# Kernel tuning notes

Hardware: AMD Instinct MI355X
Metric: run time of the kernel (lower is better)

## Reference

```python
import jax, jax.numpy as jnp
import numpy as np

B, Q, K, H = 8, 2048, 2048, 512


def setup_inputs() -> dict:
    key = jax.random.key(0)
    ks = jax.random.split(key, 12)
    s = 1.0 / np.sqrt(H)
    return {
        "query": jax.random.normal(ks[0], (B, Q, H), jnp.float32),
        "key_": jax.random.normal(ks[1], (B, K, H), jnp.float32),
        "value": jax.random.normal(ks[2], (B, K, H), jnp.float32),
        "mask": jax.random.randint(ks[3], (B, K), 0, 2).astype(bool),
        "Wq": jax.random.normal(ks[4], (H, H), jnp.float32) * s,
        "bq": jnp.zeros((H,), jnp.float32),
        "Wk": jax.random.normal(ks[5], (H, H), jnp.float32) * s,
        "bk": jnp.zeros((H,), jnp.float32),
        "Wv": jax.random.normal(ks[6], (H, H), jnp.float32) * s,
        "bv": jnp.zeros((H,), jnp.float32),
        "Wo": jax.random.normal(ks[7], (H, H), jnp.float32) * s,
        "bo": jnp.zeros((H,), jnp.float32),
    }


def reference(query, key_, value, mask, Wq, bq, Wk, bk, Wv, bv, Wo, bo):
    scale = jnp.sqrt(jnp.float32(H))
    Qp = query @ Wq + bq          # (B,Q,H)
    Kp = key_ @ Wk + bk           # (B,K,H)
    Vp = value @ Wv + bv          # (B,K,H)
    energy = jnp.einsum("bqh,bkh->bqk", Qp, Kp) / scale
    # mask is (B, key_len); torch code broadcasts it over all query rows
    energy = jnp.where(mask[:, None, :], -jnp.inf, energy)
    idx = jnp.argmax(energy, axis=-1)                 # (B,Q)
    score = jax.nn.one_hot(idx, K, dtype=energy.dtype)  # hardmax one-hot (B,Q,K)
    # score @ V is exactly a per-row gather of the argmax-selected V row
    res = jnp.take_along_axis(Vp, idx[:, :, None], axis=1)  # (B,Q,H)
    res = res @ Wo + bo
    return (res, score)
```

## Files before the change

### kernel.cpp

```cpp
#include <hip/hip_runtime.h>

typedef _Float16 f16;
typedef f16 f16x8 __attribute__((ext_vector_type(8)));
typedef f16 f16x4 __attribute__((ext_vector_type(4)));
typedef short s16x8 __attribute__((ext_vector_type(8)));
typedef short s16x4 __attribute__((ext_vector_type(4)));
typedef float f32x4 __attribute__((ext_vector_type(4)));

#define MFMA16(a,b,c)  __builtin_amdgcn_mfma_f32_16x16x32_f16(a,b,c,0,0,0)
#define MFMAB16(a,b,c) __builtin_amdgcn_mfma_f32_16x16x32_bf16(a,b,c,0,0,0)

static constexpr int Bn = 8, Qn = 2048, Kn = 2048, Hn = 512;
static constexpr int Mn = Bn * Qn;

typedef __attribute__((address_space(1))) const unsigned int as1_uint;
typedef __attribute__((address_space(3))) unsigned int as3_uint;

__device__ __forceinline__ void gl_lds16(const void* g, void* l) {
    __builtin_amdgcn_global_load_lds((as1_uint*)g, (as3_uint*)l, 16, 0, 0);
}

__device__ __forceinline__ short bf16r(float x) {
    unsigned u = __builtin_bit_cast(unsigned, x);
    u += 0x7fffu + ((u >> 16) & 1u);
    return (short)(u >> 16);
}

__device__ __forceinline__ int swz(int row) { return (row >> 1) & 3; }

__global__ __launch_bounds__(256) void prep_all(
    const int* __restrict__ mask, const float* __restrict__ Wk,
    const float* __restrict__ Wo, const float* __restrict__ bq,
    const float* __restrict__ bv, const float* __restrict__ bo,
    int* __restrict__ cidx, int* __restrict__ cnt,
    f16* __restrict__ Wk_h, f16* __restrict__ Wk_l, short* __restrict__ Wot,
    float* __restrict__ wvec, float* __restrict__ cvec)
{
    const int bid = blockIdx.x, t = threadIdx.x;
    if (bid < 8) {
        __shared__ int sums[256];
        int b = bid;
        int base = b * Kn + t * 8;
        int mv[8]; int s = 0;
        #pragma unroll
        for (int i = 0; i < 8; ++i) { mv[i] = (mask[base + i] == 0); s += mv[i]; }
        sums[t] = s;
        __syncthreads();
        for (int off = 1; off < 256; off <<= 1) {
            int v = (t >= off) ? sums[t - off] : 0;
            __syncthreads();
            sums[t] += v;
            __syncthreads();
        }
        int pos = (t > 0 ? sums[t - 1] : 0);
        #pragma unroll
        for (int i = 0; i < 8; ++i)
            if (mv[i]) cidx[b * Kn + pos++] = t * 8 + i;
        if (t == 255) {
            int total = sums[255];
            if (total == 0) { cidx[b * Kn] = 0; total = 1; }
            cnt[b] = total;
        }
    } else if (bid < 1032) {
        int e = (bid - 8) * 256 + t;
        float v = Wk[e] * 512.0f;
        f16 h = (f16)v;
        Wk_h[e] = h; Wk_l[e] = (f16)((v - (float)h) * 2048.0f);
        int r = e >> 9, c = e & 511;
        Wot[c * 512 + r] = bf16r(Wo[e]);
    } else {
        #pragma unroll
        for (int i = 0; i < 2; ++i) {
            int tt = t + i * 256;
            float s = 0.f;
            for (int n = 0; n < 512; n += 4) {
                f32x4 a = *(const f32x4*)(Wk + (size_t)tt * 512 + n);
                f32x4 q = *(const f32x4*)(bq + n);
                s += a[0]*q[0] + a[1]*q[1] + a[2]*q[2] + a[3]*q[3];
            }
            wvec[tt] = s * (1.0f / 512.0f);
            float s2 = 0.f;
            for (int h = 0; h < 512; ++h) s2 += bv[h] * Wo[h * 512 + tt];
            cvec[tt] = s2 + bo[tt];
        }
    }
}

template<int PREP>
__global__ __launch_bounds__(256) void gemm_split(
    const float* __restrict__ Af,
    const f16* __restrict__ Bh_g, const f16* __restrict__ Bl_g,
    f16* __restrict__ Oh, f16* __restrict__ Ol)
{
    __shared__ __align__(16) f16 Ah[2][2048], Al[2][2048], Bh[2][4096], Bl[2][4096];
    const int tid = threadIdx.x, lane = tid & 63, wid = tid >> 6;
    const int l15 = lane & 15, lg = lane >> 4;
    const int m0 = blockIdx.x * 64, n0 = blockIdx.y * 128;
    const int srow = lane >> 2, sg = lane & 3;
    const int ar0 = tid >> 3, ac0 = (tid & 7) * 4;

    auto stageB = [&](int buf, int ks) {
        const int k0 = ks << 5;
        #pragma unroll
        for (int h = 0; h < 2; ++h) {
            int s = wid + h * 4;
            int row = s * 16 + srow;
            int goff = k0 + ((sg ^ swz(row)) << 3);
            gl_lds16(Bh_g + (size_t)(n0 + row) * Hn + goff, &Bh[buf][s * 512]);
            gl_lds16(Bl_g + (size_t)(n0 + row) * Hn + goff, &Bl[buf][s * 512]);
        }
    };
    auto writeA = [&](int buf, const f32x4* av) {
        #pragma unroll
        for (int rr = 0; rr < 2; ++rr) {
            int row = ar0 + rr * 32;
            f16x4 oh, ol;
            #pragma unroll
            for (int j = 0; j < 4; ++j) {
                f16 hh = (f16)av[rr][j];
                oh[j] = hh;
                ol[j] = (f16)((av[rr][j] - (float)hh) * 2048.0f);
            }
            int off = row * 32 + (((ac0 >> 3) ^ swz(row)) << 3) + (ac0 & 7);
            *(f16x4*)&Ah[buf][off] = oh;
            *(f16x4*)&Al[buf][off] = ol;
        }
    };

    const float* aSrc[2];
    #pragma unroll
    for (int rr = 0; rr < 2; ++rr)
        aSrc[rr] = Af + (size_t)(m0 + ar0 + rr * 32) * Hn;

    f32x4 a0[4][2] = {}, a1[4][2] = {};
    {
        f32x4 av[2];
        #pragma unroll
        for (int rr = 0; rr < 2; ++rr) av[rr] = *(const f32x4*)(aSrc[rr] + ac0);
        stageB(0, 0);
        writeA(0, av);
    }
    __syncthreads();
    #pragma unroll 1
    for (int ks = 0; ks < 16; ++ks) {
        const int cur = ks & 1, nxt = cur ^ 1;
        f32x4 av[2];
        if (ks < 15) {
            const int k1 = (ks + 1) << 5;
            #pragma unroll
            for (int rr = 0; rr < 2; ++rr) av[rr] = *(const f32x4*)(aSrc[rr] + k1 + ac0);
            stageB(nxt, ks + 1);
        }
        f16x8 fbh[2], fbl[2];
        #pragma unroll
        for (int fj = 0; fj < 2; ++fj) {
            int row = wid * 32 + fj * 16 + l15;
            int off = row * 32 + ((lg ^ swz(row)) << 3);
            fbh[fj] = *(f16x8*)&Bh[cur][off];
            fbl[fj] = *(f16x8*)&Bl[cur][off];
        }
        #pragma unroll
        for (int fi = 0; fi < 4; ++fi) {
            int row = fi * 16 + l15;
            int off = row * 32 + ((lg ^ swz(row)) << 3);
            f16x8 fah = *(f16x8*)&Ah[cur][off];
            f16x8 fal = *(f16x8*)&Al[cur][off];
            #pragma unroll
            for (int fj = 0; fj < 2; ++fj) {
                a0[fi][fj] = MFMA16(fah, fbh[fj], a0[fi][fj]);
                a1[fi][fj] = MFMA16(fah, fbl[fj], a1[fi][fj]);
                a1[fi][fj] = MFMA16(fal, fbh[fj], a1[fi][fj]);
            }
        }
        if (ks < 15) writeA(nxt, av);
        __syncthreads();
    }
    #pragma unroll
    for (int fi = 0; fi < 4; ++fi)
    #pragma unroll
    for (int fj = 0; fj < 2; ++fj)
    #pragma unroll
    for (int j = 0; j < 4; ++j) {
        int m = m0 + fi * 16 + lg * 4 + j;
        int n = n0 + wid * 32 + fj * 16 + l15;
        float v = a0[fi][fj][j] + a1[fi][fj][j] * (1.0f / 2048.0f);
        if (PREP == 0) v *= (1.0f / 512.0f);
        f16 h = (f16)v;
        f16 lo = (f16)((v - (float)h) * 2048.0f);
        size_t o = PREP ? ((size_t)n * Hn + m) : ((size_t)m * Hn + n);
        Oh[o] = h; Ol[o] = lo;
    }
}

__global__ __launch_bounds__(256) void gemm_bfk0(
    const float* __restrict__ Af, const short* __restrict__ Bt,
    short* __restrict__ Out)
{
    __shared__ __align__(16) short As[2][2048], Bs[2][4096];
    const int tid = threadIdx.x, lane = tid & 63, wid = tid >> 6;
    const int l15 = lane & 15, lg = lane >> 4;
    const int m0 = blockIdx.x * 64, n0 = blockIdx.y * 128;
    const int srow = lane >> 2, sg = lane & 3;
    const int ar0 = tid >> 3, ac0 = (tid & 7) * 4;

    const float* aSrc[2];
    #pragma unroll
    for (int rr = 0; rr < 2; ++rr)
        aSrc[rr] = Af + (size_t)(m0 + ar0 + rr * 32) * Hn;

    auto stageB = [&](int buf, int ks) {
        const int k0 = ks << 5;
        #pragma unroll
        for (int h = 0; h < 2; ++h) {
            int s = wid + h * 4;
            int row = s * 16 + srow;
            int goff = k0 + ((sg ^ swz(row)) << 3);
            gl_lds16(Bt + (size_t)(n0 + row) * Hn + goff, &Bs[buf][s * 512]);
        }
    };
    auto writeA = [&](int buf, const f32x4* av) {
        #pragma unroll
        for (int rr = 0; rr < 2; ++rr) {
            int row = ar0 + rr * 32;
            s16x4 o;
            #pragma unroll
            for (int j = 0; j < 4; ++j) o[j] = bf16r(av[rr][j]);
            int off = row * 32 + (((ac0 >> 3) ^ swz(row)) << 3) + (ac0 & 7);
            *(s16x4*)&As[buf][off] = o;
        }
    };

    f32x4 acc[4][2] = {};
    {
        f32x4 av[2];
        #pragma unroll
        for (int rr = 0; rr < 2; ++rr) av[rr] = *(const f32x4*)(aSrc[rr] + ac0);
        stageB(0, 0);
        writeA(0, av);
    }
    __syncthreads();
    #pragma unroll 1
    for (int ks = 0; ks < 16; ++ks) {
        const int cur = ks & 1, nxt = cur ^ 1;
        f32x4 av[2];
        if (ks < 15) {
            const int k1 = (ks + 1) << 5;
            #pragma unroll
            for (int rr = 0; rr < 2; ++rr) av[rr] = *(const f32x4*)(aSrc[rr] + k1 + ac0);
            stageB(nxt, ks + 1);
        }
        s16x8 fb[2];
        #pragma unroll
        for (int fj = 0; fj < 2; ++fj) {
            int row = wid * 32 + fj * 16 + l15;
            fb[fj] = *(s16x8*)&Bs[cur][row * 32 + ((lg ^ swz(row)) << 3)];
        }
        #pragma unroll
        for (int fi = 0; fi < 4; ++fi) {
            int row = fi * 16 + l15;
            s16x8 fa = *(s16x8*)&As[cur][row * 32 + ((lg ^ swz(row)) << 3)];
            #pragma unroll
            for (int fj = 0; fj < 2; ++fj)
                acc[fi][fj] = MFMAB16(fa, fb[fj], acc[fi][fj]);
        }
        if (ks < 15) writeA(nxt, av);
        __syncthreads();
    }
    #pragma unroll
    for (int fi = 0; fi < 4; ++fi)
    #pragma unroll
    for (int fj = 0; fj < 2; ++fj)
    #pragma unroll
    for (int j = 0; j < 4; ++j) {
        int m = m0 + fi * 16 + lg * 4 + j;
        int n = n0 + wid * 32 + fj * 16 + l15;
        Out[(size_t)n * Hn + m] = bf16r(acc[fi][fj][j]);
    }
}

__global__ __launch_bounds__(256) void qm_kconv(
    const float* __restrict__ query,
    const f16* __restrict__ Mt_h, const f16* __restrict__ Mt_l,
    f16* __restrict__ qM_h, f16* __restrict__ qM_l,
    const float* __restrict__ key_, const int* __restrict__ cidx,
    const int* __restrict__ cnt, const float* __restrict__ wvec,
    f16* __restrict__ Kc_h, float* __restrict__ beta)
{
    __shared__ __align__(16) f16 smem[2][2048 + 2048 + 4096 + 4096];
    const int bid = blockIdx.x;
    const int tid = threadIdx.x, lane = tid & 63, wid = tid >> 6;
    if (bid < 1024) {
        f16 (*Ah)[2048+2048+4096+4096] = smem;
        #define AH(b,i) Ah[b][i]
        #define AL(b,i) Ah[b][2048 + (i)]
        #define BH(b,i) Ah[b][4096 + (i)]
        #define BL(b,i) Ah[b][8192 + (i)]
        const int l15 = lane & 15, lg = lane >> 4;
        const int m0 = (bid & 255) * 64, n0 = (bid >> 8) * 128;
        const int srow = lane >> 2, sg = lane & 3;
        const int ar0 = tid >> 3, ac0 = (tid & 7) * 4;

        auto stageB = [&](int buf, int ks) {
            const int k0 = ks << 5;
            #pragma unroll
            for (int h = 0; h < 2; ++h) {
                int s = wid + h * 4;
                int row = s * 16 + srow;
                int goff = k0 + ((sg ^ swz(row)) << 3);
                gl_lds16(Mt_h + (size_t)(n0 + row) * Hn + goff, &BH(buf, s * 512));
                gl_lds16(Mt_l + (size_t)(n0 + row) * Hn + goff, &BL(buf, s * 512));
            }
        };
        auto writeA = [&](int buf, const f32x4* av) {
            #pragma unroll
            for (int rr = 0; rr < 2; ++rr) {
                int row = ar0 + rr * 32;
                f16x4 oh, ol;
                #pragma unroll
                for (int j = 0; j < 4; ++j) {
                    f16 hh = (f16)av[rr][j];
                    oh[j] = hh;
                    ol[j] = (f16)((av[rr][j] - (float)hh) * 2048.0f);
                }
                int off = row * 32 + (((ac0 >> 3) ^ swz(row)) << 3) + (ac0 & 7);
                *(f16x4*)&AH(buf, off) = oh;
                *(f16x4*)&AL(buf, off) = ol;
            }
        };

        const float* aSrc[2];
        #pragma unroll
        for (int rr = 0; rr < 2; ++rr)
            aSrc[rr] = query + (size_t)(m0 + ar0 + rr * 32) * Hn;

        f32x4 a0[4][2] = {}, a1[4][2] = {};
        {
            f32x4 av[2];
            #pragma unroll
            for (int rr = 0; rr < 2; ++rr) av[rr] = *(const f32x4*)(aSrc[rr] + ac0);
            stageB(0, 0);
            writeA(0, av);
        }
        __syncthreads();
        #pragma unroll 1
        for (int ks = 0; ks < 16; ++ks) {
            const int cur = ks & 1, nxt = cur ^ 1;
            f32x4 av[2];
            if (ks < 15) {
                const int k1 = (ks + 1) << 5;
                #pragma unroll
                for (int rr = 0; rr < 2; ++rr) av[rr] = *(const f32x4*)(aSrc[rr] + k1 + ac0);
                stageB(nxt, ks + 1);
            }
            f16x8 fbh[2], fbl[2];
            #pragma unroll
            for (int fj = 0; fj < 2; ++fj) {
                int row = wid * 32 + fj * 16 + l15;
                int off = row * 32 + ((lg ^ swz(row)) << 3);
                fbh[fj] = *(f16x8*)&BH(cur, off);
                fbl[fj] = *(f16x8*)&BL(cur, off);
            }
            #pragma unroll
            for (int fi = 0; fi < 4; ++fi) {
                int row = fi * 16 + l15;
                int off = row * 32 + ((lg ^ swz(row)) << 3);
                f16x8 fah = *(f16x8*)&AH(cur, off);
                f16x8 fal = *(f16x8*)&AL(cur, off);
                #pragma unroll
                for (int fj = 0; fj < 2; ++fj) {
                    a0[fi][fj] = MFMA16(fah, fbh[fj], a0[fi][fj]);
                    a1[fi][fj] = MFMA16(fah, fbl[fj], a1[fi][fj]);
                    a1[fi][fj] = MFMA16(fal, fbh[fj], a1[fi][fj]);
                }
            }
            if (ks < 15) writeA(nxt, av);
            __syncthreads();
        }
        #pragma unroll
        for (int fi = 0; fi < 4; ++fi)
        #pragma unroll
        for (int fj = 0; fj < 2; ++fj)
        #pragma unroll
        for (int j = 0; j < 4; ++j) {
            int m = m0 + fi * 16 + lg * 4 + j;
            int n = n0 + wid * 32 + fj * 16 + l15;
            float v = (a0[fi][fj][j] + a1[fi][fj][j] * (1.0f / 2048.0f)) * (1.0f / 512.0f);
            f16 h = (f16)v;
            qM_h[(size_t)m * Hn + n] = h;
            qM_l[(size_t)m * Hn + n] = (f16)((v - (float)h) * 2048.0f);
        }
        #undef AH
        #undef AL
        #undef BH
        #undef BL
    } else {
        int kb = bid - 1024;
        int b = kb >> 9;
        int j = (kb & 511) * 4 + wid;
        int cn = cnt[b];
        if (j >= cn) return;
        const float* src = key_ + (size_t)(b * Kn + cidx[b * Kn + j]) * Hn;
        size_t dst = (size_t)(b * Kn + j) * Hn;
        float s = 0.f;
        #pragma unroll
        for (int i = 0; i < 2; ++i) {
            int c0 = lane * 8 + i * 4;
            f32x4 v = *(const f32x4*)(src + c0);
            f32x4 w = *(const f32x4*)(wvec + c0);
            f16x4 oh;
            #pragma unroll
            for (int e = 0; e < 4; ++e) {
                oh[e] = (f16)v[e];
                s += v[e] * w[e];
            }
            *(f16x4*)(Kc_h + dst + c0) = oh;
        }
        #pragma unroll
        for (int sm = 1; sm < 64; sm <<= 1) s += __shfl_xor(s, sm, 64);
        if (lane == 0) beta[b * Kn + j] = s;
    }
}

__global__ __launch_bounds__(256) void energy_approx(
    const f16* __restrict__ Qh, const f16* __restrict__ Kh,
    const float* __restrict__ beta, const int* __restrict__ cnt,
    float* __restrict__ pval1, int* __restrict__ pidx, float* __restrict__ pval2)
{
    __shared__ __align__(16) f16 Ah[2][2048], Bh[2][4096];
    const int tid = threadIdx.x, lane = tid & 63, wid = tid >> 6;
    const int l15 = lane & 15, lg = lane >> 4;
    const int qt = blockIdx.x, kc = blockIdx.y, b = blockIdx.z;
    const int cn = cnt[b];
    const int kbase = kc << 7;
    if (kbase >= cn) return;
    const int m0 = b * Qn + qt * 64;
    const int kr0 = b * Kn + kbase;
    const int srow = lane >> 2, sg = lane & 3;
    const float NEGINF = -__builtin_inff();

    auto stage = [&](int buf, int ks) {
        const int k0 = ks << 5;
        {
            int row = wid * 16 + srow;
            int goff = k0 + ((sg ^ swz(row)) << 3);
            gl_lds16(Qh + (size_t)(m0 + row) * Hn + goff, &Ah[buf][wid * 512]);
        }
        #pragma unroll
        for (int h = 0; h < 2; ++h) {
            int s = wid + h * 4;
            int row = s * 16 + srow;
            int goff = k0 + ((sg ^ swz(row)) << 3);
            gl_lds16(Kh + (size_t)(kr0 + row) * Hn + goff, &Bh[buf][s * 512]);
        }
    };

    f32x4 acc[4][2] = {};
    stage(0, 0);
    __syncthreads();
    #pragma unroll 1
    for (int ks = 0; ks < 16; ++ks) {
        const int cur = ks & 1;
        if (ks < 15) stage(cur ^ 1, ks + 1);
        f16x8 fb[2];
        #pragma unroll
        for (int fj = 0; fj < 2; ++fj) {
            int row = wid * 32 + fj * 16 + l15;
            fb[fj] = *(f16x8*)&Bh[cur][row * 32 + ((lg ^ swz(row)) << 3)];
        }
        #pragma unroll
        for (int fi = 0; fi < 4; ++fi) {
            int row = fi * 16 + l15;
            f16x8 fa = *(f16x8*)&Ah[cur][row * 32 + ((lg ^ swz(row)) << 3)];
            #pragma unroll
            for (int fj = 0; fj < 2; ++fj)
                acc[fi][fj] = MFMA16(fa, fb[fj], acc[fi][fj]);
        }
        __syncthreads();
    }
    float (*bw1)[64] = (float(*)[64])&Ah[0][0];
    int   (*bi1)[64] = (int(*)[64])&Ah[0][512];
    float (*bw2)[64] = (float(*)[64])&Ah[1][0];
    float bet[2]; int valid[2];
    #pragma unroll
    for (int fj = 0; fj < 2; ++fj) {
        int lc = wid * 32 + fj * 16 + l15;
        valid[fj] = (kbase + lc < cn);
        bet[fj] = valid[fj] ? beta[b * Kn + kbase + lc] : 0.0f;
    }
    #pragma unroll
    for (int fi = 0; fi < 4; ++fi)
    #pragma unroll
    for (int j = 0; j < 4; ++j) {
        int row = fi * 16 + lg * 4 + j;
        int lc0 = wid * 32 + l15, lc1 = lc0 + 16;
        float v0 = valid[0] ? (acc[fi][0][j] + bet[0]) : NEGINF;
        float v1 = valid[1] ? (acc[fi][1][j] + bet[1]) : NEGINF;
        float t1, t2; int ti;
        if (v1 > v0) { t1 = v1; ti = lc1; t2 = v0; }
        else         { t1 = v0; ti = lc0; t2 = v1; }
        #pragma unroll
        for (int sm = 1; sm < 16; sm <<= 1) {
            float o1 = __shfl_xor(t1, sm, 64);
            int   oi = __shfl_xor(ti, sm, 64);
            float o2 = __shfl_xor(t2, sm, 64);
            if (o1 > t1 || (o1 == t1 && oi < ti)) { t2 = fmaxf(t1, o2); t1 = o1; ti = oi; }
            else                                  { t2 = fmaxf(t2, o1); }
        }
        if (l15 == 0) { bw1[wid][row] = t1; bi1[wid][row] = ti; bw2[wid][row] = t2; }
    }
    __syncthreads();
    if (tid < 64) {
        float t1 = bw1[0][tid]; int ti = bi1[0][tid]; float t2 = bw2[0][tid];
        #pragma unroll
        for (int s = 1; s < 4; ++s) {
            float o1 = bw1[s][tid]; int oi = bi1[s][tid]; float o2 = bw2[s][tid];
            if (o1 > t1 || (o1 == t1 && oi < ti)) { t2 = fmaxf(t1, o2); t1 = o1; ti = oi; }
            else                                  { t2 = fmaxf(t2, o1); }
        }
        int m = m0 + tid;
        pval1[m * 16 + kc] = t1;
        pidx [m * 16 + kc] = kbase + ti;
        pval2[m * 16 + kc] = t2;
    }
}

__global__ __launch_bounds__(256) void refine(
    const float* __restrict__ pval1, const int* __restrict__ pidx,
    const float* __restrict__ pval2,
    const f16* __restrict__ qMh, const f16* __restrict__ qMl,
    const float* __restrict__ key_, const float* __restrict__ beta,
    const int* __restrict__ cidx, const int* __restrict__ cnt,
    int* __restrict__ idxArr)
{
    const int wid = threadIdx.x >> 6, lane = threadIdx.x & 63;
    const int m = blockIdx.x * 4 + wid;
    const int b = m >> 11;
    const int cn = cnt[b];
    const int nch = (cn + 127) >> 7;
    const float NEGINF = -__builtin_inff();

    float chv = (lane < nch) ? pval1[m * 16 + lane] : NEGINF;
    int   chi = (lane < nch) ? pidx [m * 16 + lane] : 0x7fffffff;
    float ch2 = (lane < nch) ? pval2[m * 16 + lane] : NEGINF;

    float gv = chv; int gi = chi;
    #pragma unroll
    for (int sm = 1; sm < 64; sm <<= 1) {
        float ov = __shfl_xor(gv, sm, 64);
        int   oi = __shfl_xor(gi, sm, 64);
        if (ov > gv || (ov == gv && oi < gi)) { gv = ov; gi = oi; }
    }
    const float thr = gv - 0.35f;
    unsigned long long candMask = __ballot(chv >= thr);
    unsigned long long scanMask = __ballot(ch2 >= thr);
    if (__popcll(candMask) == 1 && scanMask == 0ULL) {
        if (lane == 0) idxArr[m] = cidx[b * Kn + gi];
        return;
    }
    const f16* qhRow = qMh + (size_t)m * Hn;
    const f16* qlRow = qMl + (size_t)m * Hn;
    float bestV = NEGINF; int bestOrig = 0x7fffffff;

    auto evalLane = [&](int j) {
        int orig = cidx[b * Kn + j];
        const float* kr = key_ + ((size_t)(b * Kn + orig)) * Hn;
        float d = 0.f;
        for (int h = 0; h < 512; h += 8) {
            f16x8 qh = *(const f16x8*)(qhRow + h);
            f16x8 ql = *(const f16x8*)(qlRow + h);
            f32x4 k0 = *(const f32x4*)(kr + h);
            f32x4 k1 = *(const f32x4*)(kr + h + 4);
            #pragma unroll
            for (int e = 0; e < 4; ++e) {
                d += ((float)qh[e]     + (float)ql[e]     * (1.0f / 2048.0f)) * k0[e];
                d += ((float)qh[e + 4] + (float)ql[e + 4] * (1.0f / 2048.0f)) * k1[e];
            }
        }
        d += beta[b * Kn + j];
        if (d > bestV || (d == bestV && orig < bestOrig)) { bestV = d; bestOrig = orig; }
    };

    unsigned long long singles = candMask & ~scanMask;
    {
        int c2 = 0, myChunk = -1;
        for (int c = 0; c < nch; ++c)
            if ((singles >> c) & 1) { if (c2 == lane) myChunk = c; ++c2; }
        int mc = (myChunk >= 0) ? myChunk : 0;
        int j = __shfl(chi, mc, 64);
        if (myChunk >= 0) evalLane(j);
    }
    for (int c = 0; c < nch; ++c) {
        if (!((scanMask >> c) & 1)) continue;
        int jend = min(128, cn - c * 128);
        for (int t = lane; t < jend; t += 64) evalLane(c * 128 + t);
    }
    #pragma unroll
    for (int sm = 1; sm < 64; sm <<= 1) {
        float ov = __shfl_xor(bestV, sm, 64);
        int   oo = __shfl_xor(bestOrig, sm, 64);
        if (ov > bestV || (ov == bestV && oo < bestOrig)) { bestV = ov; bestOrig = oo; }
    }
    if (lane == 0) idxArr[m] = bestOrig;
}

__global__ __launch_bounds__(256) void tail_fused(
    const float* __restrict__ value, const short* __restrict__ NtB,
    const float* __restrict__ cvec, const int* __restrict__ idxArr,
    float* __restrict__ res, float* __restrict__ score)
{
    __shared__ __align__(16) short As[2][2048], Bs[2][4096];
    const int bid = blockIdx.x;
    const int tid = threadIdx.x, lane = tid & 63, wid = tid >> 6;
    if (bid >= 1024) {
        int m = bid - 1024;
        int c = idxArr[m];
        float* row = score + (size_t)m * Kn;
        #pragma unroll
        for (int i = 0; i < 2; ++i) {
            int v = tid + i * 256;
            f32x4 val = {0.f, 0.f, 0.f, 0.f};
            if ((c >> 2) == v) val[c & 3] = 1.0f;
            *(f32x4*)(row + v * 4) = val;
        }
        return;
    }
    const int l15 = lane & 15, lg = lane >> 4;
    const int m0 = (bid & 255) * 64, n0 = (bid >> 8) * 128;
    const int srow = lane >> 2, sg = lane & 3;
    const int ar0 = tid >> 3, ac0 = (tid & 7) * 4;

    const float* aSrc[2];
    #pragma unroll
    for (int rr = 0; rr < 2; ++rr) {
        int row = ar0 + rr * 32;
        int bb = m0 >> 11;
        aSrc[rr] = value + (size_t)(bb * Kn + idxArr[m0 + row]) * Hn;
    }

    auto stageB = [&](int buf, int ks) {
        const int k0 = ks << 5;
        #pragma unroll
        for (int h = 0; h < 2; ++h) {
            int s = wid + h * 4;
            int row = s * 16 + srow;
            int goff = k0 + ((sg ^ swz(row)) << 3);
            gl_lds16(NtB + (size_t)(n0 + row) * Hn + goff, &Bs[buf][s * 512]);
        }
    };
    auto writeA = [&](int buf, const f32x4* av) {
        #pragma unroll
        for (int rr = 0; rr < 2; ++rr) {
            int row = ar0 + rr * 32;
            s16x4 o;
            #pragma unroll
            for (int j = 0; j < 4; ++j) o[j] = bf16r(av[rr][j]);
            int off = row * 32 + (((ac0 >> 3) ^ swz(row)) << 3) + (ac0 & 7);
            *(s16x4*)&As[buf][off] = o;
        }
    };

    f32x4 acc[4][2] = {};
    {
        f32x4 av[2];
        #pragma unroll
        for (int rr = 0; rr < 2; ++rr) av[rr] = *(const f32x4*)(aSrc[rr] + ac0);
        stageB(0, 0);
        writeA(0, av);
    }
    __syncthreads();
    #pragma unroll 1
    for (int ks = 0; ks < 16; ++ks) {
        const int cur = ks & 1, nxt = cur ^ 1;
        f32x4 av[2];
        if (ks < 15) {
            const int k1 = (ks + 1) << 5;
            #pragma unroll
            for (int rr = 0; rr < 2; ++rr) av[rr] = *(const f32x4*)(aSrc[rr] + k1 + ac0);
            stageB(nxt, ks + 1);
        }
        s16x8 fb[2];
        #pragma unroll
        for (int fj = 0; fj < 2; ++fj) {
            int row = wid * 32 + fj * 16 + l15;
            fb[fj] = *(s16x8*)&Bs[cur][row * 32 + ((lg ^ swz(row)) << 3)];
        }
        #pragma unroll
        for (int fi = 0; fi < 4; ++fi) {
            int row = fi * 16 + l15;
            s16x8 fa = *(s16x8*)&As[cur][row * 32 + ((lg ^ swz(row)) << 3)];
            #pragma unroll
            for (int fj = 0; fj < 2; ++fj)
                acc[fi][fj] = MFMAB16(fa, fb[fj], acc[fi][fj]);
        }
        if (ks < 15) writeA(nxt, av);
        __syncthreads();
    }
    #pragma unroll
    for (int fi = 0; fi < 4; ++fi)
    #pragma unroll
    for (int fj = 0; fj < 2; ++fj)
    #pragma unroll
    for (int j = 0; j < 4; ++j) {
        int m = m0 + fi * 16 + lg * 4 + j;
        int n = n0 + wid * 32 + fj * 16 + l15;
        res[(size_t)m * Hn + n] = acc[fi][fj][j] + cvec[n];
    }
}

extern "C" void kernel_launch(void* const* d_in, const int* in_sizes, int n_in,
                              void* d_out, int out_size, void* d_ws, size_t ws_size,
                              hipStream_t stream)
{
    const float* query = (const float*)d_in[0];
    const float* key_  = (const float*)d_in[1];
    const float* value = (const float*)d_in[2];
    const int*   mask  = (const int*)d_in[3];
    const float* Wq = (const float*)d_in[4];
    const float* bq = (const float*)d_in[5];
    const float* Wk = (const float*)d_in[6];
    const float* bv = (const float*)d_in[9];
    const float* Wv = (const float*)d_in[8];
    const float* Wo = (const float*)d_in[10];
    const float* bo = (const float*)d_in[11];

    float* res = (float*)d_out;
    float* scoreBase = res + (size_t)Mn * Hn;
    char* sc = (char*)scoreBase;
    constexpr size_t MB = 1u << 20;
    f16*   qM_h = (f16*)(sc + 0 * MB);
    f16*   qM_l = (f16*)(sc + 16 * MB);
    f16*   Kc_h = (f16*)(sc + 32 * MB);
    char*  wb   = sc + 112 * MB;
    f16*   Mt_h = (f16*)(wb);
    f16*   Mt_l = (f16*)(wb + 524288);
    f16*   Wk_h = (f16*)(wb + 2 * 524288);
    f16*   Wk_l = (f16*)(wb + 3 * 524288);
    short* Wot  = (short*)(wb + 4 * 524288);
    float* wvec = (float*)(wb + 5 * 524288);
    float* beta = (float*)(wb + 5 * 524288 + 8192);
    int*   cidx = (int*)(wb + 5 * 524288 + 8192 + 65536);
    float* pval1 = (float*)(wb + 6 * 524288);
    int*   pidx  = (int*)(wb + 8 * 524288);
    float* pval2 = (float*)(wb + 10 * 524288);

    int*   idxArr = (int*)d_ws;
    int*   cnt    = (int*)d_ws + 16384;
    float* cvec   = (float*)((char*)d_ws + 65600);
    short* NtB    = (short*)((char*)d_ws + 67648);

    prep_all<<<1033, 256, 0, stream>>>(mask, Wk, Wo, bq, bv, bo,
                                       cidx, cnt, Wk_h, Wk_l, Wot, wvec, cvec);

    gemm_split<1><<<dim3(8, 4), 256, 0, stream>>>(Wq, Wk_h, Wk_l, Mt_h, Mt_l);
    gemm_bfk0<<<dim3(8, 4), 256, 0, stream>>>(Wv, Wot, NtB);

    qm_kconv<<<5120, 256, 0, stream>>>(query, Mt_h, Mt_l, qM_h, qM_l,
                                       key_, cidx, cnt, wvec, Kc_h, beta);

    energy_approx<<<dim3(Qn / 64, 16, Bn), 256, 0, stream>>>(
        qM_h, Kc_h, beta, cnt, pval1, pidx, pval2);

    refine<<<Mn / 4, 256, 0, stream>>>(
        pval1, pidx, pval2, qM_h, qM_l, key_, beta, cidx, cnt, idxArr);

    tail_fused<<<1024 + Mn, 256, 0, stream>>>(value, NtB, cvec, idxArr,
                                              res, scoreBase);
}
```

Before: 296.8 us.

## Apply combined Wq·Wk^T projection to compacted keys instead of queries

The composite projection matrix is now multiplied into the unmasked (compacted) keys rather than every query row, so the large split-precision GEMM only covers roughly half the rows and skips masked tiles entirely. Queries are converted to plain fp16 for the approximate energy pass, and refinement uses fp32 query against hi/lo split projected keys. The energy kernel is retiled to 128x128 blocks with a 2x2 wave layout, adding a 1/512 rescale at the epilogue. The trade-off is a different error profile in the approximate pass (unprojected fp16 query times projected fp16 key), which could change candidate selection margins.

After: 279.4 us. 5.9% less time.

```diff
diff --git a/kernel.cpp b/kernel.cpp
--- a/kernel.cpp
+++ b/kernel.cpp
@@ -78,7 +78,7 @@
                 f32x4 q = *(const f32x4*)(bq + n);
                 s += a[0]*q[0] + a[1]*q[1] + a[2]*q[2] + a[3]*q[3];
             }
-            wvec[tt] = s * (1.0f / 512.0f);
+            wvec[tt] = s;
             float s2 = 0.f;
             for (int h = 0; h < 512; ++h) s2 += bv[h] * Wo[h * 512 + tt];
             cvec[tt] = s2 + bo[tt];
@@ -86,8 +86,7 @@
     }
 }
 
-template<int PREP>
-__global__ __launch_bounds__(256) void gemm_split(
+__global__ __launch_bounds__(256) void gemm_G(
     const float* __restrict__ Af,
     const f16* __restrict__ Bh_g, const f16* __restrict__ Bl_g,
     f16* __restrict__ Oh, f16* __restrict__ Ol)
@@ -184,11 +183,9 @@
         int m = m0 + fi * 16 + lg * 4 + j;
         int n = n0 + wid * 32 + fj * 16 + l15;
         float v = a0[fi][fj][j] + a1[fi][fj][j] * (1.0f / 2048.0f);
-        if (PREP == 0) v *= (1.0f / 512.0f);
         f16 h = (f16)v;
-        f16 lo = (f16)((v - (float)h) * 2048.0f);
-        size_t o = PREP ? ((size_t)n * Hn + m) : ((size_t)m * Hn + n);
-        Oh[o] = h; Ol[o] = lo;
+        Oh[(size_t)m * Hn + n] = h;
+        Ol[(size_t)m * Hn + n] = (f16)((v - (float)h) * 2048.0f);
     }
 }
 
@@ -278,27 +275,33 @@
     }
 }
 
-__global__ __launch_bounds__(256) void qm_kconv(
-    const float* __restrict__ query,
-    const f16* __restrict__ Mt_h, const f16* __restrict__ Mt_l,
-    f16* __restrict__ qM_h, f16* __restrict__ qM_l,
-    const float* __restrict__ key_, const int* __restrict__ cidx,
-    const int* __restrict__ cnt, const float* __restrict__ wvec,
-    f16* __restrict__ Kc_h, float* __restrict__ beta)
+__global__ __launch_bounds__(256) void kmqb(
+    const float* __restrict__ key_, const float* __restrict__ query,
+    const f16* __restrict__ G_h, const f16* __restrict__ G_l,
+    const int* __restrict__ cidx, const int* __restrict__ cnt,
+    const float* __restrict__ wvec,
+    f16* __restrict__ kM_h, f16* __restrict__ kM_l,
+    f16* __restrict__ qf, float* __restrict__ beta)
 {
-    __shared__ __align__(16) f16 smem[2][2048 + 2048 + 4096 + 4096];
+    __shared__ __align__(16) f16 Ah[2][2048], Al[2][2048], Bh[2][4096], Bl[2][4096];
     const int bid = blockIdx.x;
     const int tid = threadIdx.x, lane = tid & 63, wid = tid >> 6;
     if (bid < 1024) {
-        f16 (*Ah)[2048+2048+4096+4096] = smem;
-        #define AH(b,i) Ah[b][i]
-        #define AL(b,i) Ah[b][2048 + (i)]
-        #define BH(b,i) Ah[b][4096 + (i)]
-        #define BL(b,i) Ah[b][8192 + (i)]
+        const int b = bid >> 7, rem = bid & 127;
+        const int m0l = (rem >> 2) * 64, n0 = (rem & 3) * 128;
+        const int cn = cnt[b];
+        if (m0l >= cn) return;
         const int l15 = lane & 15, lg = lane >> 4;
-        const int m0 = (bid & 255) * 64, n0 = (bid >> 8) * 128;
         const int srow = lane >> 2, sg = lane & 3;
         const int ar0 = tid >> 3, ac0 = (tid & 7) * 4;
+
+        const float* aSrc[2];
+        #pragma unroll
+        for (int rr = 0; rr < 2; ++rr) {
+            int r = m0l + ar0 + rr * 32;
+            int cid = (r < cn) ? cidx[b * Kn + r] : 0;
+            aSrc[rr] = key_ + (size_t)(b * Kn + cid) * Hn;
+        }
 
         auto stageB = [&](int buf, int ks) {
             const int k0 = ks << 5;
@@ -307,8 +310,8 @@
                 int s = wid + h * 4;
                 int row = s * 16 + srow;
                 int goff = k0 + ((sg ^ swz(row)) << 3);
-                gl_lds16(Mt_h + (size_t)(n0 + row) * Hn + goff, &BH(buf, s * 512));
-                gl_lds16(Mt_l + (size_t)(n0 + row) * Hn + goff, &BL(buf, s * 512));
+                gl_lds16(G_h + (size_t)(n0 + row) * Hn + goff, &Bh[buf][s * 512]);
+                gl_lds16(G_l + (size_t)(n0 + row) * Hn + goff, &Bl[buf][s * 512]);
             }
         };
         auto writeA = [&](int buf, const f32x4* av) {
@@ -323,15 +326,10 @@
                     ol[j] = (f16)((av[rr][j] - (float)hh) * 2048.0f);
                 }
                 int off = row * 32 + (((ac0 >> 3) ^ swz(row)) << 3) + (ac0 & 7);
-                *(f16x4*)&AH(buf, off) = oh;
-                *(f16x4*)&AL(buf, off) = ol;
+                *(f16x4*)&Ah[buf][off] = oh;
+                *(f16x4*)&Al[buf][off] = ol;
             }
         };
-
-        const float* aSrc[2];
-        #pragma unroll
-        for (int rr = 0; rr < 2; ++rr)
-            aSrc[rr] = query + (size_t)(m0 + ar0 + rr * 32) * Hn;
 
         f32x4 a0[4][2] = {}, a1[4][2] = {};
         {
@@ -357,15 +355,15 @@
             for (int fj = 0; fj < 2; ++fj) {
                 int row = wid * 32 + fj * 16 + l15;
                 int off = row * 32 + ((lg ^ swz(row)) << 3);
-                fbh[fj] = *(f16x8*)&BH(cur, off);
-                fbl[fj] = *(f16x8*)&BL(cur, off);
+                fbh[fj] = *(f16x8*)&Bh[cur][off];
+                fbl[fj] = *(f16x8*)&Bl[cur][off];
             }
             #pragma unroll
             for (int fi = 0; fi < 4; ++fi) {
                 int row = fi * 16 + l15;
                 int off = row * 32 + ((lg ^ swz(row)) << 3);
-                f16x8 fah = *(f16x8*)&AH(cur, off);
-                f16x8 fal = *(f16x8*)&AL(cur, off);
+                f16x8 fah = *(f16x8*)&Ah[cur][off];
+                f16x8 fal = *(f16x8*)&Al[cur][off];
                 #pragma unroll
                 for (int fj = 0; fj < 2; ++fj) {
                     a0[fi][fj] = MFMA16(fah, fbh[fj], a0[fi][fj]);
@@ -382,122 +380,115 @@
         for (int fj = 0; fj < 2; ++fj)
         #pragma unroll
         for (int j = 0; j < 4; ++j) {
-            int m = m0 + fi * 16 + lg * 4 + j;
+            int jr = m0l + fi * 16 + lg * 4 + j;
             int n = n0 + wid * 32 + fj * 16 + l15;
-            float v = (a0[fi][fj][j] + a1[fi][fj][j] * (1.0f / 2048.0f)) * (1.0f / 512.0f);
+            float v = a0[fi][fj][j] + a1[fi][fj][j] * (1.0f / 2048.0f);
             f16 h = (f16)v;
-            qM_h[(size_t)m * Hn + n] = h;
-            qM_l[(size_t)m * Hn + n] = (f16)((v - (float)h) * 2048.0f);
-        }
-        #undef AH
-        #undef AL
-        #undef BH
-        #undef BL
+            kM_h[((size_t)(b * Kn + jr)) * Hn + n] = h;
+            kM_l[((size_t)(b * Kn + jr)) * Hn + n] = (f16)((v - (float)h) * 2048.0f);
+        }
+    } else if (bid < 5120) {
+        int m = (bid - 1024) * 4 + wid;
+        const float* src = query + (size_t)m * Hn + lane * 8;
+        f32x4 v0 = *(const f32x4*)(src);
+        f32x4 v1 = *(const f32x4*)(src + 4);
+        f16x8 o;
+        #pragma unroll
+        for (int e = 0; e < 4; ++e) { o[e] = (f16)v0[e]; o[e + 4] = (f16)v1[e]; }
+        *(f16x8*)(qf + (size_t)m * Hn + lane * 8) = o;
     } else {
-        int kb = bid - 1024;
-        int b = kb >> 9;
-        int j = (kb & 511) * 4 + wid;
-        int cn = cnt[b];
-        if (j >= cn) return;
+        int s = (bid - 5120) * 4 + wid;
+        int b = s >> 11, j = s & 2047;
+        if (j >= cnt[b]) return;
         const float* src = key_ + (size_t)(b * Kn + cidx[b * Kn + j]) * Hn;
-        size_t dst = (size_t)(b * Kn + j) * Hn;
-        float s = 0.f;
+        float acc = 0.f;
         #pragma unroll
         for (int i = 0; i < 2; ++i) {
             int c0 = lane * 8 + i * 4;
             f32x4 v = *(const f32x4*)(src + c0);
             f32x4 w = *(const f32x4*)(wvec + c0);
-            f16x4 oh;
-            #pragma unroll
-            for (int e = 0; e < 4; ++e) {
-                oh[e] = (f16)v[e];
-                s += v[e] * w[e];
-            }
-            *(f16x4*)(Kc_h + dst + c0) = oh;
-        }
-        #pragma unroll
-        for (int sm = 1; sm < 64; sm <<= 1) s += __shfl_xor(s, sm, 64);
-        if (lane == 0) beta[b * Kn + j] = s;
+            acc += v[0]*w[0] + v[1]*w[1] + v[2]*w[2] + v[3]*w[3];
+        }
+        #pragma unroll
+        for (int sm = 1; sm < 64; sm <<= 1) acc += __shfl_xor(acc, sm, 64);
+        if (lane == 0) beta[b * Kn + j] = acc;
     }
 }
 
 __global__ __launch_bounds__(256) void energy_approx(
-    const f16* __restrict__ Qh, const f16* __restrict__ Kh,
+    const f16* __restrict__ qf, const f16* __restrict__ kMh,
     const float* __restrict__ beta, const int* __restrict__ cnt,
     float* __restrict__ pval1, int* __restrict__ pidx, float* __restrict__ pval2)
 {
-    __shared__ __align__(16) f16 Ah[2][2048], Bh[2][4096];
+    __shared__ __align__(16) f16 Ah[2][4096], Bh[2][4096];
     const int tid = threadIdx.x, lane = tid & 63, wid = tid >> 6;
-    const int l15 = lane & 15, lg = lane >> 4;
+    const int wr = wid >> 1, wc = wid & 1, l15 = lane & 15, lg = lane >> 4;
     const int qt = blockIdx.x, kc = blockIdx.y, b = blockIdx.z;
     const int cn = cnt[b];
     const int kbase = kc << 7;
     if (kbase >= cn) return;
-    const int m0 = b * Qn + qt * 64;
+    const int m0 = b * Qn + qt * 128;
     const int kr0 = b * Kn + kbase;
     const int srow = lane >> 2, sg = lane & 3;
     const float NEGINF = -__builtin_inff();
 
     auto stage = [&](int buf, int ks) {
         const int k0 = ks << 5;
-        {
-            int row = wid * 16 + srow;
-            int goff = k0 + ((sg ^ swz(row)) << 3);
-            gl_lds16(Qh + (size_t)(m0 + row) * Hn + goff, &Ah[buf][wid * 512]);
-        }
         #pragma unroll
         for (int h = 0; h < 2; ++h) {
             int s = wid + h * 4;
             int row = s * 16 + srow;
             int goff = k0 + ((sg ^ swz(row)) << 3);
-            gl_lds16(Kh + (size_t)(kr0 + row) * Hn + goff, &Bh[buf][s * 512]);
+            gl_lds16(qf  + (size_t)(m0 + row) * Hn + goff, &Ah[buf][s * 512]);
+            gl_lds16(kMh + (size_t)(kr0 + row) * Hn + goff, &Bh[buf][s * 512]);
         }
     };
 
-    f32x4 acc[4][2] = {};
+    f32x4 acc[4][4] = {};
     stage(0, 0);
     __syncthreads();
     #pragma unroll 1
     for (int ks = 0; ks < 16; ++ks) {
         const int cur = ks & 1;
         if (ks < 15) stage(cur ^ 1, ks + 1);
-        f16x8 fb[2];
-        #pragma unroll
-        for (int fj = 0; fj < 2; ++fj) {
-            int row = wid * 32 + fj * 16 + l15;
+        f16x8 fb[4];
+        #pragma unroll
+        for (int fj = 0; fj < 4; ++fj) {
+            int row = wc * 64 + fj * 16 + l15;
             fb[fj] = *(f16x8*)&Bh[cur][row * 32 + ((lg ^ swz(row)) << 3)];
         }
         #pragma unroll
         for (int fi = 0; fi < 4; ++fi) {
-            int row = fi * 16 + l15;
+            int row = wr * 64 + fi * 16 + l15;
             f16x8 fa = *(f16x8*)&Ah[cur][row * 32 + ((lg ^ swz(row)) << 3)];
             #pragma unroll
-            for (int fj = 0; fj < 2; ++fj)
+            for (int fj = 0; fj < 4; ++fj)
                 acc[fi][fj] = MFMA16(fa, fb[fj], acc[fi][fj]);
         }
         __syncthreads();
     }
-    float (*bw1)[64] = (float(*)[64])&Ah[0][0];
-    int   (*bi1)[64] = (int(*)[64])&Ah[0][512];
-    float (*bw2)[64] = (float(*)[64])&Ah[1][0];
-    float bet[2]; int valid[2];
-    #pragma unroll
-    for (int fj = 0; fj < 2; ++fj) {
-        int lc = wid * 32 + fj * 16 + l15;
+    float bet[4]; int valid[4];
+    #pragma unroll
+    for (int fj = 0; fj < 4; ++fj) {
+        int lc = wc * 64 + fj * 16 + l15;
         valid[fj] = (kbase + lc < cn);
         bet[fj] = valid[fj] ? beta[b * Kn + kbase + lc] : 0.0f;
     }
+    float (*bw1)[128] = (float(*)[128])((char*)&Ah[0][0]);
+    int   (*bi1)[128] = (int(*)[128])((char*)&Ah[0][0] + 1024);
+    float (*bw2)[128] = (float(*)[128])((char*)&Ah[0][0] + 2048);
     #pragma unroll
     for (int fi = 0; fi < 4; ++fi)
     #pragma unroll
     for (int j = 0; j < 4; ++j) {
-        int row = fi * 16 + lg * 4 + j;
-        int lc0 = wid * 32 + l15, lc1 = lc0 + 16;
-        float v0 = valid[0] ? (acc[fi][0][j] + bet[0]) : NEGINF;
-        float v1 = valid[1] ? (acc[fi][1][j] + bet[1]) : NEGINF;
-        float t1, t2; int ti;
-        if (v1 > v0) { t1 = v1; ti = lc1; t2 = v0; }
-        else         { t1 = v0; ti = lc0; t2 = v1; }
+        float t1 = NEGINF, t2 = NEGINF; int ti = 0x7fffffff;
+        #pragma unroll
+        for (int fj = 0; fj < 4; ++fj) {
+            int lc = wc * 64 + fj * 16 + l15;
+            float v = valid[fj] ? (acc[fi][fj][j] * (1.0f / 512.0f) + bet[fj]) : NEGINF;
+            if (v > t1 || (v == t1 && lc < ti)) { t2 = t1; t1 = v; ti = lc; }
+            else t2 = fmaxf(t2, v);
+        }
         #pragma unroll
         for (int sm = 1; sm < 16; sm <<= 1) {
             float o1 = __shfl_xor(t1, sm, 64);
@@ -506,17 +497,17 @@
             if (o1 > t1 || (o1 == t1 && oi < ti)) { t2 = fmaxf(t1, o2); t1 = o1; ti = oi; }
             else                                  { t2 = fmaxf(t2, o1); }
         }
-        if (l15 == 0) { bw1[wid][row] = t1; bi1[wid][row] = ti; bw2[wid][row] = t2; }
+        if (l15 == 0) {
+            int row = wr * 64 + fi * 16 + lg * 4 + j;
+            bw1[wc][row] = t1; bi1[wc][row] = ti; bw2[wc][row] = t2;
+        }
     }
     __syncthreads();
-    if (tid < 64) {
+    if (tid < 128) {
         float t1 = bw1[0][tid]; int ti = bi1[0][tid]; float t2 = bw2[0][tid];
-        #pragma unroll
-        for (int s = 1; s < 4; ++s) {
-            float o1 = bw1[s][tid]; int oi = bi1[s][tid]; float o2 = bw2[s][tid];
-            if (o1 > t1 || (o1 == t1 && oi < ti)) { t2 = fmaxf(t1, o2); t1 = o1; ti = oi; }
-            else                                  { t2 = fmaxf(t2, o1); }
-        }
+        float o1 = bw1[1][tid]; int oi = bi1[1][tid]; float o2 = bw2[1][tid];
+        if (o1 > t1 || (o1 == t1 && oi < ti)) { t2 = fmaxf(t1, o2); t1 = o1; ti = oi; }
+        else                                  { t2 = fmaxf(t2, o1); }
         int m = m0 + tid;
         pval1[m * 16 + kc] = t1;
         pidx [m * 16 + kc] = kbase + ti;
@@ -527,8 +518,9 @@
 __global__ __launch_bounds__(256) void refine(
     const float* __restrict__ pval1, const int* __restrict__ pidx,
     const float* __restrict__ pval2,
-    const f16* __restrict__ qMh, const f16* __restrict__ qMl,
-    const float* __restrict__ key_, const float* __restrict__ beta,
+    const float* __restrict__ query,
+    const f16* __restrict__ kMh, const f16* __restrict__ kMl,
+    const float* __restrict__ beta,
     const int* __restrict__ cidx, const int* __restrict__ cnt,
     int* __restrict__ idxArr)
 {
@@ -557,26 +549,26 @@
         if (lane == 0) idxArr[m] = cidx[b * Kn + gi];
         return;
     }
-    const f16* qhRow = qMh + (size_t)m * Hn;
-    const f16* qlRow = qMl + (size_t)m * Hn;
+    const float* qr = query + (size_t)m * Hn;
     float bestV = NEGINF; int bestOrig = 0x7fffffff;
 
     auto evalLane = [&](int j) {
-        int orig = cidx[b * Kn + j];
-        const float* kr = key_ + ((size_t)(b * Kn + orig)) * Hn;
+        const f16* kh = kMh + ((size_t)(b * Kn + j)) * Hn;
+        const f16* kl = kMl + ((size_t)(b * Kn + j)) * Hn;
         float d = 0.f;
         for (int h = 0; h < 512; h += 8) {
-            f16x8 qh = *(const f16x8*)(qhRow + h);
-            f16x8 ql = *(const f16x8*)(qlRow + h);
-            f32x4 k0 = *(const f32x4*)(kr + h);
-            f32x4 k1 = *(const f32x4*)(kr + h + 4);
+            f32x4 q0 = *(const f32x4*)(qr + h);
+            f32x4 q1 = *(const f32x4*)(qr + h + 4);
+            f16x8 vh = *(const f16x8*)(kh + h);
+            f16x8 vl = *(const f16x8*)(kl + h);
             #pragma unroll
             for (int e = 0; e < 4; ++e) {
-                d += ((float)qh[e]     + (float)ql[e]     * (1.0f / 2048.0f)) * k0[e];
-                d += ((float)qh[e + 4] + (float)ql[e + 4] * (1.0f / 2048.0f)) * k1[e];
-            }
-        }
-        d += beta[b * Kn + j];
+                d += q0[e] * ((float)vh[e]     + (float)vl[e]     * (1.0f / 2048.0f));
+                d += q1[e] * ((float)vh[e + 4] + (float)vl[e + 4] * (1.0f / 2048.0f));
+            }
+        }
+        d = d * (1.0f / 512.0f) + beta[b * Kn + j];
+        int orig = cidx[b * Kn + j];
         if (d > bestV || (d == bestV && orig < bestOrig)) { bestV = d; bestOrig = orig; }
     };
 
@@ -727,12 +719,12 @@
     float* scoreBase = res + (size_t)Mn * Hn;
     char* sc = (char*)scoreBase;
     constexpr size_t MB = 1u << 20;
-    f16*   qM_h = (f16*)(sc + 0 * MB);
-    f16*   qM_l = (f16*)(sc + 16 * MB);
-    f16*   Kc_h = (f16*)(sc + 32 * MB);
+    f16*   qf   = (f16*)(sc + 0 * MB);
+    f16*   kM_h = (f16*)(sc + 16 * MB);
+    f16*   kM_l = (f16*)(sc + 32 * MB);
     char*  wb   = sc + 112 * MB;
-    f16*   Mt_h = (f16*)(wb);
-    f16*   Mt_l = (f16*)(wb + 524288);
+    f16*   G_h  = (f16*)(wb);
+    f16*   G_l  = (f16*)(wb + 524288);
     f16*   Wk_h = (f16*)(wb + 2 * 524288);
     f16*   Wk_l = (f16*)(wb + 3 * 524288);
     short* Wot  = (short*)(wb + 4 * 524288);
@@ -751,17 +743,17 @@
     prep_all<<<1033, 256, 0, stream>>>(mask, Wk, Wo, bq, bv, bo,
                                        cidx, cnt, Wk_h, Wk_l, Wot, wvec, cvec);
 
-    gemm_split<1><<<dim3(8, 4), 256, 0, stream>>>(Wq, Wk_h, Wk_l, Mt_h, Mt_l);
+    gemm_G<<<dim3(8, 4), 256, 0, stream>>>(Wq, Wk_h, Wk_l, G_h, G_l);
     gemm_bfk0<<<dim3(8, 4), 256, 0, stream>>>(Wv, Wot, NtB);
 
-    qm_kconv<<<5120, 256, 0, stream>>>(query, Mt_h, Mt_l, qM_h, qM_l,
-                                       key_, cidx, cnt, wvec, Kc_h, beta);
-
-    energy_approx<<<dim3(Qn / 64, 16, Bn), 256, 0, stream>>>(
-        qM_h, Kc_h, beta, cnt, pval1, pidx, pval2);
+    kmqb<<<9216, 256, 0, stream>>>(key_, query, G_h, G_l, cidx, cnt, wvec,
+                                   kM_h, kM_l, qf, beta);
+
+    energy_approx<<<dim3(Qn / 128, 16, Bn), 256, 0, stream>>>(
+        qf, kM_h, beta, cnt, pval1, pidx, pval2);
 
     refine<<<Mn / 4, 256, 0, stream>>>(
-        pval1, pidx, pval2, qM_h, qM_l, key_, beta, cidx, cnt, idxArr);
+        pval1, pidx, pval2, query, kM_h, kM_l, beta, cidx, cnt, idxArr);
 
     tail_fused<<<1024 + Mn, 256, 0, stream>>>(value, NtB, cvec, idxArr,
                                               res, scoreBase);
```
